# Kernel optimization log

Measured on AMD Instinct MI355X. Metric: run time of the kernel, lower is better.

Reference implementation:

```python
import jax, jax.numpy as jnp
import numpy as np

NUM_FIELDS = 26
VOCAB = 100000
B = 16384
D = 64            # embedding_dim
BM1, BM2 = 128, 64    # bottom_mlp_sizes
TM1, TM2 = 256, 1     # top mlp hidden/out (top_mlp_sizes=[512,256,1] -> Linear(415,256),ReLU,Linear(256,1))
NUM_FEATS = NUM_FIELDS + 1
NUM_INTER = NUM_FEATS * (NUM_FEATS - 1) // 2   # 351
TOP_IN = NUM_INTER + BM2                        # 415


def setup_inputs() -> dict:
    key = jax.random.key(0)
    ks = jax.random.split(key, 13)
    x_cat = jax.random.randint(ks[0], (NUM_FIELDS, B), 0, VOCAB)
    price = jax.random.normal(ks[1], (B,), dtype=jnp.float32)
    emb_tables = jax.random.normal(ks[2], (NUM_FIELDS, VOCAB, D), dtype=jnp.float32) * 0.05
    Wp = jax.random.normal(ks[3], (1, D), dtype=jnp.float32) * 0.1
    bp = jnp.zeros((D,), jnp.float32)
    W1 = jax.random.normal(ks[4], (D, BM1), dtype=jnp.float32) * 0.1
    b1 = jnp.zeros((BM1,), jnp.float32)
    W2 = jax.random.normal(ks[5], (BM1, BM2), dtype=jnp.float32) * 0.1
    b2 = jnp.zeros((BM2,), jnp.float32)
    Wt1 = jax.random.normal(ks[6], (TOP_IN, TM1), dtype=jnp.float32) * 0.05
    bt1 = jnp.zeros((TM1,), jnp.float32)
    Wt2 = jax.random.normal(ks[7], (TM1, TM2), dtype=jnp.float32) * 0.05
    bt2 = jnp.zeros((TM2,), jnp.float32)
    return {"x_cat": x_cat, "price": price, "emb_tables": emb_tables,
            "Wp": Wp, "bp": bp, "W1": W1, "b1": b1, "W2": W2, "b2": b2,
            "Wt1": Wt1, "bt1": bt1, "Wt2": Wt2, "bt2": bt2}


# precomputed upper-triangular (i<j, row-major) index pairs -- matches the torch double loop order
_IU, _JU = np.triu_indices(NUM_FEATS, k=1)


def reference(x_cat, price, emb_tables, Wp, bp, W1, b1, W2, b2, Wt1, bt1, Wt2, bt2):
    # embedding gathers: [F, B, D] -> [B, F, D]
    emb = emb_tables[jnp.arange(NUM_FIELDS)[:, None], x_cat]
    emb = jnp.transpose(emb, (1, 0, 2))
    # dense (price) projection: [B, D]
    dense_embed = price[:, None] @ Wp + bp
    # all features: [B, F+1, D]
    feats = jnp.concatenate([emb, dense_embed[:, None, :]], axis=1)
    # pairwise dot products via batched Gram matrix, then triangular gather
    gram = jnp.einsum('bid,bjd->bij', feats, feats)          # [B, 27, 27]
    interactions = gram[:, _IU, _JU]                          # [B, 351]
    # bottom MLP on dense embedding
    h = jax.nn.relu(dense_embed @ W1 + b1)
    dense_out = jax.nn.relu(h @ W2 + b2)                      # [B, 64]
    # top MLP
    concat = jnp.concatenate([interactions, dense_out], axis=1)  # [B, 415]
    t = jax.nn.relu(concat @ Wt1 + bt1)
    out = (t @ Wt2 + bt2)[:, 0]                               # [B]
    return out
```

## Files before the change

kernel.cpp:

```cpp
#include <hip/hip_runtime.h>
#include <hip/hip_bf16.h>
#include <cstdint>

#define NUM_FIELDS 26
#define VOCAB      100000
#define BATCH      16384
#define CK         416

typedef __attribute__((ext_vector_type(8)))  short bf16x8_t;
typedef __attribute__((ext_vector_type(16))) float f32x16_t;

__device__ __forceinline__ short f2bf(float x) {
  unsigned u = __builtin_bit_cast(unsigned, x);
  u += 0x7FFFu + ((u >> 16) & 1u);
  return (short)(u >> 16);
}

__global__ void k0_prepare(const float* __restrict__ Wp, const float* __restrict__ bp,
                           const float* __restrict__ W1, const float* __restrict__ b1,
                           const float* __restrict__ W2, const float* __restrict__ b2,
                           float* __restrict__ bps, float* __restrict__ PQ) {
  __shared__ float u1s[128], c1s[128], ts[128];
  __shared__ int ord[128];
  const int j = threadIdx.x;
  float u = 0.f, c = 0.f;
  for (int d = 0; d < 64; ++d) {
    float w = W1[d * 128 + j];
    u = fmaf(Wp[d], w, u);
    c = fmaf(bp[d], w, c);
  }
  c += b1[j];
  u1s[j] = u; c1s[j] = c;
  ts[j] = (u != 0.f) ? (-c / u) : __builtin_inff();
  __syncthreads();
  const float tj = ts[j];
  int r = 0;
  for (int i = 0; i < 128; ++i) {
    float ti = ts[i];
    if (ti < tj || (ti == tj && i < j)) ++r;
  }
  ord[r] = j;
  __syncthreads();
  bps[j] = ts[ord[j]];
  if (j < 64) {
    const int d = j;
    float P = 0.f, Q = b2[d];
    for (int k = 0; k < 128; ++k) {
      float uk = u1s[k];
      bool act = (uk < 0.f) || (uk == 0.f && c1s[k] > 0.f);
      if (act) {
        float w = W2[k * 64 + d];
        P = fmaf(uk, w, P);
        Q = fmaf(c1s[k], w, Q);
      }
    }
    PQ[d] = P; PQ[129 * 64 + d] = Q;
    for (int seg = 1; seg <= 128; ++seg) {
      int jk = ord[seg - 1];
      float uk = u1s[jk], ck = c1s[jk];
      float sgn = (uk > 0.f) ? 1.f : ((uk < 0.f) ? -1.f : 0.f);
      float w = W2[jk * 64 + d] * sgn;
      P = fmaf(uk, w, P);
      Q = fmaf(ck, w, Q);
      PQ[seg * 64 + d] = P;
      PQ[129 * 64 + seg * 64 + d] = Q;
    }
  }
}

__global__ __launch_bounds__(64) void k0b_wt1t(const float* __restrict__ Wt1,
                                               short* __restrict__ wt1t) {
  const int n = blockIdx.x;
  for (int k = threadIdx.x; k < CK; k += 64) {
    float v = (k < 415) ? Wt1[(size_t)k * 256 + n] : 0.f;
    wt1t[(size_t)n * CK + k] = f2bf(v);
  }
}

__global__ __launch_bounds__(256) void k1_features(
    const int* __restrict__ x_cat, const float* __restrict__ price,
    const float* __restrict__ emb, const float* __restrict__ Wp,
    const float* __restrict__ bp, const float* __restrict__ bps_g,
    const float* __restrict__ PQ, short* __restrict__ concat) {
  __shared__ __align__(16) short Fb[4][32 * 72];
  __shared__ __align__(16) short Cs[4][CK];
  __shared__ float bps_s[128];
  const int tid = threadIdx.x, lane = tid & 63, w = tid >> 6;
  if (tid < 128) bps_s[tid] = bps_g[tid];
  {
    int* zp = (int*)&Fb[w][27 * 72];
    for (int i = lane; i < 180; i += 64) zp[i] = 0;
  }
  const int s = blockIdx.x * 4 + w;
  const float pr = price[s];
  int idxv = 0;
  if (lane < NUM_FIELDS) idxv = x_cat[lane * BATCH + s];
  const int r16 = lane >> 4, c4 = (lane & 15) * 4;
  #pragma unroll
  for (int g = 0; g < 6; ++g) {
    const int r = g * 4 + r16;
    const int idx = __shfl(idxv, r, 64);
    const float4 v = *(const float4*)&emb[((size_t)r * VOCAB + idx) * 64 + c4];
    union { short s4[4]; uint2 u; } t;
    t.s4[0] = f2bf(v.x); t.s4[1] = f2bf(v.y); t.s4[2] = f2bf(v.z); t.s4[3] = f2bf(v.w);
    *(uint2*)&Fb[w][r * 72 + c4] = t.u;
  }
  {
    const int r = 24 + ((lane >> 4) & 1);
    const int idx = __shfl(idxv, r, 64);
    if (lane < 32) {
      const float4 v = *(const float4*)&emb[((size_t)r * VOCAB + idx) * 64 + c4];
      union { short s4[4]; uint2 u; } t;
      t.s4[0] = f2bf(v.x); t.s4[1] = f2bf(v.y); t.s4[2] = f2bf(v.z); t.s4[3] = f2bf(v.w);
      *(uint2*)&Fb[w][r * 72 + c4] = t.u;
    }
  }
  Fb[w][26 * 72 + lane] = f2bf(fmaf(pr, Wp[lane], bp[lane]));
  __syncthreads();
  const int row = lane & 31, koff = (lane >> 5) * 8;
  bf16x8_t a0 = *(const bf16x8_t*)&Fb[w][row * 72 +  0 + koff];
  bf16x8_t a1 = *(const bf16x8_t*)&Fb[w][row * 72 + 16 + koff];
  bf16x8_t a2 = *(const bf16x8_t*)&Fb[w][row * 72 + 32 + koff];
  bf16x8_t a3 = *(const bf16x8_t*)&Fb[w][row * 72 + 48 + koff];
  f32x16_t acc = {0.f,0.f,0.f,0.f,0.f,0.f,0.f,0.f,0.f,0.f,0.f,0.f,0.f,0.f,0.f,0.f};
  acc = __builtin_amdgcn_mfma_f32_32x32x16_bf16(a0, a0, acc, 0, 0, 0);
  acc = __builtin_amdgcn_mfma_f32_32x32x16_bf16(a1, a1, acc, 0, 0, 0);
  acc = __builtin_amdgcn_mfma_f32_32x32x16_bf16(a2, a2, acc, 0, 0, 0);
  acc = __builtin_amdgcn_mfma_f32_32x32x16_bf16(a3, a3, acc, 0, 0, 0);
  int lo = 0, hi = 128;
  while (lo < hi) { int mid = (lo + hi) >> 1; if (bps_s[mid] < pr) lo = mid + 1; else hi = mid; }
  float dv = fmaf(pr, PQ[lo * 64 + lane], PQ[129 * 64 + lo * 64 + lane]);
  dv = fmaxf(dv, 0.f);
  Cs[w][351 + lane] = f2bf(dv);
  if (lane == 0) Cs[w][415] = 0;
  const int jc = row, rh = (lane >> 5) * 4;
  #pragma unroll
  for (int reg = 0; reg < 16; ++reg) {
    int i = (reg & 3) + 8 * (reg >> 2) + rh;
    if (i < jc && jc < 27) {
      int p = 26 * i - (i * (i - 1)) / 2 + (jc - i - 1);
      Cs[w][p] = f2bf(acc[reg]);
    }
  }
  __syncthreads();
  if (lane < 52) {
    *(uint4*)&concat[(size_t)s * CK + lane * 8] = ((const uint4*)Cs[w])[lane];
  }
}

__global__ __launch_bounds__(256) void k2_top(const short* __restrict__ concat,
    const short* __restrict__ wt1t, const float* __restrict__ bt1,
    const float* __restrict__ Wt2, const float* __restrict__ bt2,
    float* __restrict__ out) {
  __shared__ float partial_s[4][32];
  const int tid = threadIdx.x, lane = tid & 63, w = tid >> 6;
  const int m0 = blockIdx.x * 32;
  const int row = lane & 31, kh = lane >> 5;
  const short* ap  = concat + (size_t)(m0 + row) * CK + kh * 8;
  const int nb = w * 64;
  const short* bp0 = wt1t + (size_t)(nb + row) * CK + kh * 8;
  const short* bp1 = bp0 + (size_t)32 * CK;
  f32x16_t acc0 = {0.f,0.f,0.f,0.f,0.f,0.f,0.f,0.f,0.f,0.f,0.f,0.f,0.f,0.f,0.f,0.f};
  f32x16_t acc1 = acc0;
  #pragma unroll
  for (int k0 = 0; k0 < CK; k0 += 16) {
    bf16x8_t a  = *(const bf16x8_t*)(ap + k0);
    bf16x8_t b0 = *(const bf16x8_t*)(bp0 + k0);
    bf16x8_t b1 = *(const bf16x8_t*)(bp1 + k0);
    acc0 = __builtin_amdgcn_mfma_f32_32x32x16_bf16(a, b0, acc0, 0, 0, 0);
    acc1 = __builtin_amdgcn_mfma_f32_32x32x16_bf16(a, b1, acc1, 0, 0, 0);
  }
  const int n0 = nb + row;
  const float bt1a = bt1[n0], bt1b = bt1[n0 + 32];
  const float w2a  = Wt2[n0], w2b  = Wt2[n0 + 32];
  float ps[16];
  #pragma unroll
  for (int r = 0; r < 16; ++r) {
    float v0 = fmaxf(acc0[r] + bt1a, 0.f) * w2a;
    float v1 = fmaxf(acc1[r] + bt1b, 0.f) * w2b;
    ps[r] = v0 + v1;
  }
  #pragma unroll
  for (int d = 1; d <= 16; d <<= 1) {
    #pragma unroll
    for (int r = 0; r < 16; ++r) ps[r] += __shfl_xor(ps[r], d, 64);
  }
  if (row == 0) {
    const int rh = kh * 4;
    #pragma unroll
    for (int r = 0; r < 16; ++r)
      partial_s[w][(r & 3) + 8 * (r >> 2) + rh] = ps[r];
  }
  __syncthreads();
  if (tid < 32)
    out[m0 + tid] = partial_s[0][tid] + partial_s[1][tid] +
                    partial_s[2][tid] + partial_s[3][tid] + bt2[0];
}

extern "C" void kernel_launch(void* const* d_in, const int* in_sizes, int n_in,
                              void* d_out, int out_size, void* d_ws, size_t ws_size,
                              hipStream_t stream) {
  const int*   x_cat = (const int*)d_in[0];
  const float* price = (const float*)d_in[1];
  const float* emb   = (const float*)d_in[2];
  const float* Wp    = (const float*)d_in[3];
  const float* bp    = (const float*)d_in[4];
  const float* W1    = (const float*)d_in[5];
  const float* b1    = (const float*)d_in[6];
  const float* W2    = (const float*)d_in[7];
  const float* b2    = (const float*)d_in[8];
  const float* Wt1   = (const float*)d_in[9];
  const float* bt1   = (const float*)d_in[10];
  const float* Wt2   = (const float*)d_in[11];
  const float* bt2   = (const float*)d_in[12];
  float* out = (float*)d_out;

  float* ws     = (float*)d_ws;
  float* PQ     = ws;
  float* bps    = ws + 16512;
  short* concat = (short*)(ws + 16640);
  short* wt1t   = concat + (size_t)BATCH * CK;

  k0_prepare<<<dim3(1),   dim3(128), 0, stream>>>(Wp, bp, W1, b1, W2, b2, bps, PQ);
  k0b_wt1t  <<<dim3(256), dim3(64),  0, stream>>>(Wt1, wt1t);
  k1_features<<<dim3(BATCH / 4), dim3(256), 0, stream>>>(x_cat, price, emb, Wp, bp, bps, PQ, concat);
  k2_top     <<<dim3(BATCH / 32), dim3(256), 0, stream>>>(concat, wt1t, bt1, Wt2, bt2, out);
}
```

Baseline: 826.1 us.

## Fuse feature interaction and top MLP into one kernel, merge prep kernels

Merges the two preparation kernels into one launch, with block 0 building the piecewise-linear bottom-MLP tables and the other blocks transposing Wt1 to bf16. Fuses the gather/Gram interaction kernel with the top-MLP GEMM so each 512-thread block builds 32 concat rows in shared memory and immediately multiplies them by Wt1. This removes the global round-trip of the concat buffer and two launches. In exchange each wave processes four samples serially, blocks use more shared memory, and the kernel depends on the ordering between the Fb writes and the MFMA reads within a wave.

New measurement: 812.2 us. Within noise of the previous version (-1.7%).

```diff
diff --git a/kernel.cpp b/kernel.cpp
--- a/kernel.cpp
+++ b/kernel.cpp
@@ -6,6 +6,7 @@
 #define VOCAB      100000
 #define BATCH      16384
 #define CK         416
+#define CS_STRIDE  424
 
 typedef __attribute__((ext_vector_type(8)))  short bf16x8_t;
 typedef __attribute__((ext_vector_type(16))) float f32x16_t;
@@ -16,10 +17,20 @@
   return (short)(u >> 16);
 }
 
-__global__ void k0_prepare(const float* __restrict__ Wp, const float* __restrict__ bp,
-                           const float* __restrict__ W1, const float* __restrict__ b1,
-                           const float* __restrict__ W2, const float* __restrict__ b2,
-                           float* __restrict__ bps, float* __restrict__ PQ) {
+__global__ __launch_bounds__(128) void k0_prep(
+    const float* __restrict__ Wp, const float* __restrict__ bp,
+    const float* __restrict__ W1, const float* __restrict__ b1,
+    const float* __restrict__ W2, const float* __restrict__ b2,
+    const float* __restrict__ Wt1,
+    float* __restrict__ bps, float* __restrict__ PQ, short* __restrict__ wt1t) {
+  if (blockIdx.x != 0) {
+    const int n = blockIdx.x - 1;
+    for (int k = threadIdx.x; k < CK; k += 128) {
+      float v = (k < 415) ? Wt1[(size_t)k * 256 + n] : 0.f;
+      wt1t[(size_t)n * CK + k] = f2bf(v);
+    }
+    return;
+  }
   __shared__ float u1s[128], c1s[128], ts[128];
   __shared__ int ord[128];
   const int j = threadIdx.x;
@@ -68,22 +79,16 @@
   }
 }
 
-__global__ __launch_bounds__(64) void k0b_wt1t(const float* __restrict__ Wt1,
-                                               short* __restrict__ wt1t) {
-  const int n = blockIdx.x;
-  for (int k = threadIdx.x; k < CK; k += 64) {
-    float v = (k < 415) ? Wt1[(size_t)k * 256 + n] : 0.f;
-    wt1t[(size_t)n * CK + k] = f2bf(v);
-  }
-}
-
-__global__ __launch_bounds__(256) void k1_features(
+__global__ __launch_bounds__(512, 4) void k1_fused(
     const int* __restrict__ x_cat, const float* __restrict__ price,
     const float* __restrict__ emb, const float* __restrict__ Wp,
-    const float* __restrict__ bp, const float* __restrict__ bps_g,
-    const float* __restrict__ PQ, short* __restrict__ concat) {
-  __shared__ __align__(16) short Fb[4][32 * 72];
-  __shared__ __align__(16) short Cs[4][CK];
+    const float* __restrict__ bp_, const float* __restrict__ bps_g,
+    const float* __restrict__ PQ, const short* __restrict__ wt1t,
+    const float* __restrict__ bt1, const float* __restrict__ Wt2,
+    const float* __restrict__ bt2, float* __restrict__ out) {
+  __shared__ __align__(16) short Fb[8][32 * 72];
+  __shared__ __align__(16) short Cs[32][CS_STRIDE];
+  __shared__ float partial_s[8][32];
   __shared__ float bps_s[128];
   const int tid = threadIdx.x, lane = tid & 63, w = tid >> 6;
   if (tid < 128) bps_s[tid] = bps_g[tid];
@@ -91,110 +96,94 @@
     int* zp = (int*)&Fb[w][27 * 72];
     for (int i = lane; i < 180; i += 64) zp[i] = 0;
   }
-  const int s = blockIdx.x * 4 + w;
-  const float pr = price[s];
-  int idxv = 0;
-  if (lane < NUM_FIELDS) idxv = x_cat[lane * BATCH + s];
+  __syncthreads();
+  const float wpv = Wp[lane], bpv = bp_[lane];
   const int r16 = lane >> 4, c4 = (lane & 15) * 4;
-  #pragma unroll
-  for (int g = 0; g < 6; ++g) {
-    const int r = g * 4 + r16;
-    const int idx = __shfl(idxv, r, 64);
-    const float4 v = *(const float4*)&emb[((size_t)r * VOCAB + idx) * 64 + c4];
-    union { short s4[4]; uint2 u; } t;
-    t.s4[0] = f2bf(v.x); t.s4[1] = f2bf(v.y); t.s4[2] = f2bf(v.z); t.s4[3] = f2bf(v.w);
-    *(uint2*)&Fb[w][r * 72 + c4] = t.u;
-  }
-  {
-    const int r = 24 + ((lane >> 4) & 1);
-    const int idx = __shfl(idxv, r, 64);
-    if (lane < 32) {
+  const int row = lane & 31, kh = lane >> 5;
+  const int koff = kh * 8;
+  for (int it = 0; it < 4; ++it) {
+    const int sm = w * 4 + it;
+    const int s = blockIdx.x * 32 + sm;
+    const float pr = price[s];
+    int idxv = 0;
+    if (lane < NUM_FIELDS) idxv = x_cat[lane * BATCH + s];
+    #pragma unroll
+    for (int g = 0; g < 6; ++g) {
+      const int r = g * 4 + r16;
+      const int idx = __shfl(idxv, r, 64);
       const float4 v = *(const float4*)&emb[((size_t)r * VOCAB + idx) * 64 + c4];
       union { short s4[4]; uint2 u; } t;
       t.s4[0] = f2bf(v.x); t.s4[1] = f2bf(v.y); t.s4[2] = f2bf(v.z); t.s4[3] = f2bf(v.w);
       *(uint2*)&Fb[w][r * 72 + c4] = t.u;
     }
-  }
-  Fb[w][26 * 72 + lane] = f2bf(fmaf(pr, Wp[lane], bp[lane]));
-  __syncthreads();
-  const int row = lane & 31, koff = (lane >> 5) * 8;
-  bf16x8_t a0 = *(const bf16x8_t*)&Fb[w][row * 72 +  0 + koff];
-  bf16x8_t a1 = *(const bf16x8_t*)&Fb[w][row * 72 + 16 + koff];
-  bf16x8_t a2 = *(const bf16x8_t*)&Fb[w][row * 72 + 32 + koff];
-  bf16x8_t a3 = *(const bf16x8_t*)&Fb[w][row * 72 + 48 + koff];
-  f32x16_t acc = {0.f,0.f,0.f,0.f,0.f,0.f,0.f,0.f,0.f,0.f,0.f,0.f,0.f,0.f,0.f,0.f};
-  acc = __builtin_amdgcn_mfma_f32_32x32x16_bf16(a0, a0, acc, 0, 0, 0);
-  acc = __builtin_amdgcn_mfma_f32_32x32x16_bf16(a1, a1, acc, 0, 0, 0);
-  acc = __builtin_amdgcn_mfma_f32_32x32x16_bf16(a2, a2, acc, 0, 0, 0);
-  acc = __builtin_amdgcn_mfma_f32_32x32x16_bf16(a3, a3, acc, 0, 0, 0);
-  int lo = 0, hi = 128;
-  while (lo < hi) { int mid = (lo + hi) >> 1; if (bps_s[mid] < pr) lo = mid + 1; else hi = mid; }
-  float dv = fmaf(pr, PQ[lo * 64 + lane], PQ[129 * 64 + lo * 64 + lane]);
-  dv = fmaxf(dv, 0.f);
-  Cs[w][351 + lane] = f2bf(dv);
-  if (lane == 0) Cs[w][415] = 0;
-  const int jc = row, rh = (lane >> 5) * 4;
-  #pragma unroll
-  for (int reg = 0; reg < 16; ++reg) {
-    int i = (reg & 3) + 8 * (reg >> 2) + rh;
-    if (i < jc && jc < 27) {
-      int p = 26 * i - (i * (i - 1)) / 2 + (jc - i - 1);
-      Cs[w][p] = f2bf(acc[reg]);
-    }
-  }
-  __syncthreads();
-  if (lane < 52) {
-    *(uint4*)&concat[(size_t)s * CK + lane * 8] = ((const uint4*)Cs[w])[lane];
-  }
-}
-
-__global__ __launch_bounds__(256) void k2_top(const short* __restrict__ concat,
-    const short* __restrict__ wt1t, const float* __restrict__ bt1,
-    const float* __restrict__ Wt2, const float* __restrict__ bt2,
-    float* __restrict__ out) {
-  __shared__ float partial_s[4][32];
-  const int tid = threadIdx.x, lane = tid & 63, w = tid >> 6;
-  const int m0 = blockIdx.x * 32;
-  const int row = lane & 31, kh = lane >> 5;
-  const short* ap  = concat + (size_t)(m0 + row) * CK + kh * 8;
-  const int nb = w * 64;
-  const short* bp0 = wt1t + (size_t)(nb + row) * CK + kh * 8;
-  const short* bp1 = bp0 + (size_t)32 * CK;
-  f32x16_t acc0 = {0.f,0.f,0.f,0.f,0.f,0.f,0.f,0.f,0.f,0.f,0.f,0.f,0.f,0.f,0.f,0.f};
-  f32x16_t acc1 = acc0;
+    {
+      const int r = 24 + (r16 & 1);
+      const int idx = __shfl(idxv, r, 64);
+      if (lane < 32) {
+        const float4 v = *(const float4*)&emb[((size_t)r * VOCAB + idx) * 64 + c4];
+        union { short s4[4]; uint2 u; } t;
+        t.s4[0] = f2bf(v.x); t.s4[1] = f2bf(v.y); t.s4[2] = f2bf(v.z); t.s4[3] = f2bf(v.w);
+        *(uint2*)&Fb[w][r * 72 + c4] = t.u;
+      }
+    }
+    Fb[w][26 * 72 + lane] = f2bf(fmaf(pr, wpv, bpv));
+    bf16x8_t a0 = *(const bf16x8_t*)&Fb[w][row * 72 +  0 + koff];
+    bf16x8_t a1 = *(const bf16x8_t*)&Fb[w][row * 72 + 16 + koff];
+    bf16x8_t a2 = *(const bf16x8_t*)&Fb[w][row * 72 + 32 + koff];
+    bf16x8_t a3 = *(const bf16x8_t*)&Fb[w][row * 72 + 48 + koff];
+    f32x16_t acc = {0.f,0.f,0.f,0.f,0.f,0.f,0.f,0.f,0.f,0.f,0.f,0.f,0.f,0.f,0.f,0.f};
+    acc = __builtin_amdgcn_mfma_f32_32x32x16_bf16(a0, a0, acc, 0, 0, 0);
+    acc = __builtin_amdgcn_mfma_f32_32x32x16_bf16(a1, a1, acc, 0, 0, 0);
+    acc = __builtin_amdgcn_mfma_f32_32x32x16_bf16(a2, a2, acc, 0, 0, 0);
+    acc = __builtin_amdgcn_mfma_f32_32x32x16_bf16(a3, a3, acc, 0, 0, 0);
+    int lo = 0, hi = 128;
+    while (lo < hi) { int mid = (lo + hi) >> 1; if (bps_s[mid] < pr) lo = mid + 1; else hi = mid; }
+    float dv = fmaf(pr, PQ[lo * 64 + lane], PQ[129 * 64 + lo * 64 + lane]);
+    dv = fmaxf(dv, 0.f);
+    Cs[sm][351 + lane] = f2bf(dv);
+    if (lane == 0) Cs[sm][415] = 0;
+    const int jc = row, rh = kh * 4;
+    #pragma unroll
+    for (int reg = 0; reg < 16; ++reg) {
+      int i = (reg & 3) + 8 * (reg >> 2) + rh;
+      if (i < jc && jc < 27) {
+        int p = 26 * i - (i * (i - 1)) / 2 + (jc - i - 1);
+        Cs[sm][p] = f2bf(acc[reg]);
+      }
+    }
+  }
+  __syncthreads();
+  const int n0 = w * 32;
+  const short* bp0 = wt1t + (size_t)(n0 + row) * CK + koff;
+  f32x16_t tacc = {0.f,0.f,0.f,0.f,0.f,0.f,0.f,0.f,0.f,0.f,0.f,0.f,0.f,0.f,0.f,0.f};
   #pragma unroll
   for (int k0 = 0; k0 < CK; k0 += 16) {
-    bf16x8_t a  = *(const bf16x8_t*)(ap + k0);
-    bf16x8_t b0 = *(const bf16x8_t*)(bp0 + k0);
-    bf16x8_t b1 = *(const bf16x8_t*)(bp1 + k0);
-    acc0 = __builtin_amdgcn_mfma_f32_32x32x16_bf16(a, b0, acc0, 0, 0, 0);
-    acc1 = __builtin_amdgcn_mfma_f32_32x32x16_bf16(a, b1, acc1, 0, 0, 0);
-  }
-  const int n0 = nb + row;
-  const float bt1a = bt1[n0], bt1b = bt1[n0 + 32];
-  const float w2a  = Wt2[n0], w2b  = Wt2[n0 + 32];
+    bf16x8_t a = *(const bf16x8_t*)&Cs[row][k0 + koff];
+    bf16x8_t b = *(const bf16x8_t*)(bp0 + k0);
+    tacc = __builtin_amdgcn_mfma_f32_32x32x16_bf16(a, b, tacc, 0, 0, 0);
+  }
+  const int n = n0 + row;
+  const float bt1v = bt1[n], w2v = Wt2[n];
   float ps[16];
   #pragma unroll
-  for (int r = 0; r < 16; ++r) {
-    float v0 = fmaxf(acc0[r] + bt1a, 0.f) * w2a;
-    float v1 = fmaxf(acc1[r] + bt1b, 0.f) * w2b;
-    ps[r] = v0 + v1;
-  }
+  for (int r = 0; r < 16; ++r) ps[r] = fmaxf(tacc[r] + bt1v, 0.f) * w2v;
   #pragma unroll
   for (int d = 1; d <= 16; d <<= 1) {
     #pragma unroll
     for (int r = 0; r < 16; ++r) ps[r] += __shfl_xor(ps[r], d, 64);
   }
   if (row == 0) {
-    const int rh = kh * 4;
     #pragma unroll
     for (int r = 0; r < 16; ++r)
-      partial_s[w][(r & 3) + 8 * (r >> 2) + rh] = ps[r];
-  }
-  __syncthreads();
-  if (tid < 32)
-    out[m0 + tid] = partial_s[0][tid] + partial_s[1][tid] +
-                    partial_s[2][tid] + partial_s[3][tid] + bt2[0];
+      partial_s[w][(r & 3) + 8 * (r >> 2) + 4 * kh] = ps[r];
+  }
+  __syncthreads();
+  if (tid < 32) {
+    float ssum = bt2[0];
+    #pragma unroll
+    for (int ww = 0; ww < 8; ++ww) ssum += partial_s[ww][tid];
+    out[blockIdx.x * 32 + tid] = ssum;
+  }
 }
 
 extern "C" void kernel_launch(void* const* d_in, const int* in_sizes, int n_in,
@@ -215,14 +204,12 @@
   const float* bt2   = (const float*)d_in[12];
   float* out = (float*)d_out;
 
-  float* ws     = (float*)d_ws;
-  float* PQ     = ws;
-  float* bps    = ws + 16512;
-  short* concat = (short*)(ws + 16640);
-  short* wt1t   = concat + (size_t)BATCH * CK;
-
-  k0_prepare<<<dim3(1),   dim3(128), 0, stream>>>(Wp, bp, W1, b1, W2, b2, bps, PQ);
-  k0b_wt1t  <<<dim3(256), dim3(64),  0, stream>>>(Wt1, wt1t);
-  k1_features<<<dim3(BATCH / 4), dim3(256), 0, stream>>>(x_cat, price, emb, Wp, bp, bps, PQ, concat);
-  k2_top     <<<dim3(BATCH / 32), dim3(256), 0, stream>>>(concat, wt1t, bt1, Wt2, bt2, out);
-}
+  float* ws   = (float*)d_ws;
+  float* PQ   = ws;
+  float* bps  = ws + 16512;
+  short* wt1t = (short*)(ws + 16640);
+
+  k0_prep <<<dim3(257), dim3(128), 0, stream>>>(Wp, bp, W1, b1, W2, b2, Wt1, bps, PQ, wt1t);
+  k1_fused<<<dim3(BATCH / 32), dim3(512), 0, stream>>>(x_cat, price, emb, Wp, bp,
+                                                       bps, PQ, wt1t, bt1, Wt2, bt2, out);
+}
```
